# Optimization experiments

Hardware: AMD Instinct MI355X
Metric: run time of the kernel (lower is better)

Reference implementation:

```python
import jax, jax.numpy as jnp
import numpy as np

DIM = 512
HEADS = 8
DIM_HEAD = 64
INNER = HEADS * DIM_HEAD
SCALE = DIM_HEAD ** -0.5


def setup_inputs() -> dict:
    key = jax.random.key(0)
    ks = jax.random.split(key, 6)
    b, n = 2, 2048
    x = jax.random.normal(ks[0], (b, n, DIM), dtype=jnp.float32)
    # torch Linear(dim, 3*inner, bias=False): store as [in, out] for x @ W
    w_qkv = jax.random.normal(ks[1], (DIM, 3 * INNER), dtype=jnp.float32) * (DIM ** -0.5)
    # Conv2d(heads, heads, 1, bias=False) weights squeezed to [out_h, in_h]
    w_pre = jax.random.normal(ks[2], (HEADS, HEADS), dtype=jnp.float32) * (HEADS ** -0.5)
    w_post = jax.random.normal(ks[3], (HEADS, HEADS), dtype=jnp.float32) * (HEADS ** -0.5)
    w_out = jax.random.normal(ks[4], (INNER, DIM), dtype=jnp.float32) * (INNER ** -0.5)
    b_out = jax.random.normal(ks[5], (DIM,), dtype=jnp.float32) * 0.01
    return {"x": x, "w_qkv": w_qkv, "w_pre": w_pre, "w_post": w_post,
            "w_out": w_out, "b_out": b_out}


def reference(x, w_qkv, w_pre, w_post, w_out, b_out):
    b, n, _ = x.shape
    qkv = x @ w_qkv  # [b, n, 3*inner]
    q, k, v = jnp.split(qkv, 3, axis=-1)
    # b n (h d) -> b h n d
    split_heads = lambda t: t.reshape(b, n, HEADS, DIM_HEAD).transpose(0, 2, 1, 3)
    q, k, v = split_heads(q), split_heads(k), split_heads(v)
    dots = jnp.einsum('bhid,bhjd->bhij', q, k) * SCALE
    # pre-softmax talking-heads: 1x1 conv over the head axis
    dots = jnp.einsum('gh,bhij->bgij', w_pre, dots)
    attn = jax.nn.softmax(dots, axis=-1)
    # post-softmax talking-heads mix
    attn = jnp.einsum('gh,bhij->bgij', w_post, attn)
    out = jnp.einsum('bhij,bhjd->bhid', attn, v)
    out = out.transpose(0, 2, 1, 3).reshape(b, n, INNER)  # b h n d -> b n (h d)
    return out @ w_out + b_out
```

## Files before the change

### kernel.cpp

```cpp
#include <hip/hip_runtime.h>
#include <hip/hip_bf16.h>

typedef unsigned short ushort_t;
typedef __attribute__((ext_vector_type(8))) short short8;
typedef __attribute__((ext_vector_type(4))) short short4v;
typedef __attribute__((ext_vector_type(4))) float floatx4;

#define MFMA16(a, b, c) __builtin_amdgcn_mfma_f32_16x16x32_bf16(a, b, c, 0, 0, 0)

__device__ __forceinline__ float bf2f(ushort_t u) {
    unsigned int v = ((unsigned int)u) << 16;
    return __int_as_float((int)v);
}
__device__ __forceinline__ ushort_t f2bf(float f) {
    unsigned int x = (unsigned int)__float_as_int(f);
    unsigned int r = (x + 0x7FFFu + ((x >> 16) & 1u)) >> 16;
    return (ushort_t)r;
}

__global__ __launch_bounds__(256) void k_cvt(const floatx4* __restrict__ src,
                                             short4v* __restrict__ dst, int n4) {
    int i = blockIdx.x * 256 + threadIdx.x;
    if (i < n4) {
        floatx4 v = src[i];
        short4v o;
        o[0] = (short)f2bf(v[0]);
        o[1] = (short)f2bf(v[1]);
        o[2] = (short)f2bf(v[2]);
        o[3] = (short)f2bf(v[3]);
        dst[i] = o;
    }
}

__global__ __launch_bounds__(256) void k_transpose_cvt(const float* __restrict__ src,
                                                       ushort_t* __restrict__ dst, int R, int C) {
    __shared__ float t[32][33];
    int tx = threadIdx.x & 31, ty = threadIdx.x >> 5;
    int r0 = blockIdx.y * 32, c0 = blockIdx.x * 32;
    for (int y = ty; y < 32; y += 8) t[y][tx] = src[(r0 + y) * C + c0 + tx];
    __syncthreads();
    for (int y = ty; y < 32; y += 8) dst[(c0 + y) * R + r0 + tx] = f2bf(t[tx][y]);
}

__global__ __launch_bounds__(256) void k_qkv(const ushort_t* __restrict__ x,
                                             const ushort_t* __restrict__ wt,
                                             ushort_t* __restrict__ qs,
                                             ushort_t* __restrict__ ks,
                                             ushort_t* __restrict__ vt) {
    const int tid = threadIdx.x, lane = tid & 63, wv = tid >> 6;
    const int col = lane & 15, quad = lane >> 4;
    const int row0 = blockIdx.y * 64 + (wv >> 1) * 32;
    const int c0 = blockIdx.x * 64 + (wv & 1) * 32;
    floatx4 acc[2][2];
#pragma unroll
    for (int i = 0; i < 2; i++)
#pragma unroll
        for (int j = 0; j < 2; j++) acc[i][j] = (floatx4){0.f, 0.f, 0.f, 0.f};
    for (int k0 = 0; k0 < 512; k0 += 32) {
        const int ko = k0 + quad * 8;
        short8 a0 = *(const short8*)&x[(row0 + col) * 512 + ko];
        short8 a1 = *(const short8*)&x[(row0 + 16 + col) * 512 + ko];
        short8 b0 = *(const short8*)&wt[(c0 + col) * 512 + ko];
        short8 b1 = *(const short8*)&wt[(c0 + 16 + col) * 512 + ko];
        acc[0][0] = MFMA16(a0, b0, acc[0][0]);
        acc[0][1] = MFMA16(a0, b1, acc[0][1]);
        acc[1][0] = MFMA16(a1, b0, acc[1][0]);
        acc[1][1] = MFMA16(a1, b1, acc[1][1]);
    }
#pragma unroll
    for (int i = 0; i < 2; i++)
#pragma unroll
        for (int j = 0; j < 2; j++)
#pragma unroll
            for (int r = 0; r < 4; r++) {
                int row = row0 + i * 16 + quad * 4 + r;
                int c = c0 + j * 16 + col;
                float v = acc[i][j][r];
                int bb = row >> 11, n = row & 2047;
                int which = c >> 9, hh = (c >> 6) & 7, d = c & 63;
                int hidx = bb * 8 + hh;
                if (which == 0)
                    qs[(hidx * 2048 + n) * 64 + d] = f2bf(v * 0.125f);
                else if (which == 1)
                    ks[(hidx * 2048 + n) * 64 + d] = f2bf(v);
                else
                    vt[(hidx * 64 + d) * 2048 + n] = f2bf(v);
            }
}

__global__ __launch_bounds__(512) void k_attn(const ushort_t* __restrict__ qs,
                                              const ushort_t* __restrict__ ks,
                                              const ushort_t* __restrict__ vt,
                                              const float* __restrict__ w_pre,
                                              const float* __restrict__ w_post,
                                              const ushort_t* __restrict__ wot,
                                              const float* __restrict__ bias,
                                              float* __restrict__ out) {
    __shared__ __align__(16) ushort_t qlds[8 * 16 * 72];
    __shared__ __align__(16) ushort_t amix[8 * 16 * 136];
    __shared__ __align__(16) ushort_t oline[16 * 520];
    __shared__ float wbuf[128];
    __shared__ float red[8][8][16][2];
    __shared__ float clds[8][16];
    const int tid = threadIdx.x, lane = tid & 63, wv = tid >> 6;
    const int col = lane & 15, quad = lane >> 4;
    const int b = blockIdx.y, n0 = blockIdx.x * 16;

    if (tid < 64) wbuf[tid] = w_pre[tid];
    else if (tid < 128) wbuf[tid] = w_post[tid - 64];
    for (int c = tid; c < 1024; c += 512) {
        int hh = c >> 7, rem = c & 127, ii = rem >> 3, dc = (rem & 7) * 8;
        *(short8*)&qlds[(hh * 16 + ii) * 72 + dc] =
            *(const short8*)&qs[((b * 8 + hh) * 2048 + n0 + ii) * 64 + dc];
    }
    __syncthreads();

    float M[8][4], L[8][4];
#pragma unroll
    for (int g = 0; g < 8; g++)
#pragma unroll
        for (int r = 0; r < 4; r++) { M[g][r] = -1e30f; L[g][r] = 0.f; }
    for (int jt = 0; jt < 16; jt++) {
        const int jw = jt * 128 + wv * 16;
        floatx4 S[8];
#pragma unroll
        for (int h = 0; h < 8; h++) {
            const ushort_t* qb = &qlds[(h * 16 + col) * 72 + quad * 8];
            short8 a0 = *(const short8*)&qb[0];
            short8 a1 = *(const short8*)&qb[32];
            const ushort_t* kb = &ks[((b * 8 + h) * 2048 + jw + col) * 64 + quad * 8];
            short8 b0 = *(const short8*)&kb[0];
            short8 b1 = *(const short8*)&kb[32];
            floatx4 a = (floatx4){0.f, 0.f, 0.f, 0.f};
            a = MFMA16(a0, b0, a);
            a = MFMA16(a1, b1, a);
            S[h] = a;
        }
#pragma unroll
        for (int g = 0; g < 8; g++)
#pragma unroll
            for (int r = 0; r < 4; r++) {
                float s = 0.f;
#pragma unroll
                for (int h = 0; h < 8; h++) s = fmaf(wbuf[g * 8 + h], S[h][r], s);
                float Mn = fmaxf(M[g][r], s);
                L[g][r] = L[g][r] * __expf(M[g][r] - Mn) + __expf(s - Mn);
                M[g][r] = Mn;
            }
    }
#pragma unroll
    for (int g = 0; g < 8; g++)
#pragma unroll
        for (int r = 0; r < 4; r++) {
            float M0 = M[g][r], L0 = L[g][r];
#pragma unroll
            for (int k = 1; k < 16; k <<= 1) {
                float Mo = __shfl_xor(M0, k, 64);
                float Lo = __shfl_xor(L0, k, 64);
                float Mn = fmaxf(M0, Mo);
                L0 = L0 * __expf(M0 - Mn) + Lo * __expf(Mo - Mn);
                M0 = Mn;
            }
            if (col == 0) { red[wv][g][quad * 4 + r][0] = M0; red[wv][g][quad * 4 + r][1] = L0; }
        }
    __syncthreads();
    if (tid < 128) {
        int g = tid >> 4, ii = tid & 15;
        float m = -1e30f;
#pragma unroll
        for (int w2 = 0; w2 < 8; w2++) m = fmaxf(m, red[w2][g][ii][0]);
        float l = 0.f;
#pragma unroll
        for (int w2 = 0; w2 < 8; w2++) l += red[w2][g][ii][1] * __expf(red[w2][g][ii][0] - m);
        clds[g][ii] = m + __logf(fmaxf(l, 1e-30f));
    }
    __syncthreads();
    float cr[8][4];
#pragma unroll
    for (int g = 0; g < 8; g++)
#pragma unroll
        for (int r = 0; r < 4; r++) cr[g][r] = clds[g][quad * 4 + r];

    floatx4 O[4];
#pragma unroll
    for (int nt = 0; nt < 4; nt++) O[nt] = (floatx4){0.f, 0.f, 0.f, 0.f};
    const int e = wv;
    for (int jt = 0; jt < 16; jt++) {
        const int j0 = jt * 128;
        const int jw = j0 + wv * 16;
        floatx4 S[8];
#pragma unroll
        for (int h = 0; h < 8; h++) {
            const ushort_t* qb = &qlds[(h * 16 + col) * 72 + quad * 8];
            short8 a0 = *(const short8*)&qb[0];
            short8 a1 = *(const short8*)&qb[32];
            const ushort_t* kb = &ks[((b * 8 + h) * 2048 + jw + col) * 64 + quad * 8];
            short8 b0 = *(const short8*)&kb[0];
            short8 b1 = *(const short8*)&kb[32];
            floatx4 a = (floatx4){0.f, 0.f, 0.f, 0.f};
            a = MFMA16(a0, b0, a);
            a = MFMA16(a1, b1, a);
            S[h] = a;
        }
        float P[8][4];
#pragma unroll
        for (int g = 0; g < 8; g++)
#pragma unroll
            for (int r = 0; r < 4; r++) {
                float s = 0.f;
#pragma unroll
                for (int h = 0; h < 8; h++) s = fmaf(wbuf[g * 8 + h], S[h][r], s);
                P[g][r] = __expf(fminf(s - cr[g][r], 30.f));
            }
#pragma unroll
        for (int e2 = 0; e2 < 8; e2++)
#pragma unroll
            for (int r = 0; r < 4; r++) {
                float a = 0.f;
#pragma unroll
                for (int g = 0; g < 8; g++) a = fmaf(wbuf[64 + e2 * 8 + g], P[g][r], a);
                amix[(e2 * 16 + quad * 4 + r) * 136 + wv * 16 + col] = f2bf(a);
            }
        __syncthreads();
#pragma unroll
        for (int nt = 0; nt < 4; nt++) {
            floatx4 a = O[nt];
#pragma unroll
            for (int k2 = 0; k2 < 4; k2++) {
                short8 af = *(const short8*)&amix[(e * 16 + col) * 136 + k2 * 32 + quad * 8];
                short8 bf = *(const short8*)&vt[((b * 8 + e) * 64 + nt * 16 + col) * 2048 + j0 +
                                                k2 * 32 + quad * 8];
                a = MFMA16(af, bf, a);
            }
            O[nt] = a;
        }
        __syncthreads();
    }
#pragma unroll
    for (int nt = 0; nt < 4; nt++)
#pragma unroll
        for (int r = 0; r < 4; r++)
            oline[(quad * 4 + r) * 520 + e * 64 + nt * 16 + col] = f2bf(O[nt][r]);
    __syncthreads();
#pragma unroll
    for (int nt = 0; nt < 4; nt++) {
        floatx4 acc = (floatx4){0.f, 0.f, 0.f, 0.f};
        const int c = wv * 64 + nt * 16 + col;
#pragma unroll
        for (int k2 = 0; k2 < 16; k2++) {
            short8 af = *(const short8*)&oline[col * 520 + k2 * 32 + quad * 8];
            short8 bf = *(const short8*)&wot[c * 512 + k2 * 32 + quad * 8];
            acc = MFMA16(af, bf, acc);
        }
        float bz = bias[c];
#pragma unroll
        for (int r = 0; r < 4; r++)
            out[(b * 2048 + n0 + quad * 4 + r) * 512 + c] = acc[r] + bz;
    }
}

extern "C" void kernel_launch(void* const* d_in, const int* in_sizes, int n_in,
                              void* d_out, int out_size, void* d_ws, size_t ws_size,
                              hipStream_t stream) {
    const float* x = (const float*)d_in[0];
    const float* w_qkv = (const float*)d_in[1];
    const float* w_pre = (const float*)d_in[2];
    const float* w_post = (const float*)d_in[3];
    const float* w_out = (const float*)d_in[4];
    const float* b_out = (const float*)d_in[5];
    char* ws = (char*)d_ws;
    ushort_t* qs = (ushort_t*)(ws);
    ushort_t* ks = (ushort_t*)(ws + (4u << 20));
    ushort_t* vt = (ushort_t*)(ws + (8u << 20));
    ushort_t* xb = (ushort_t*)(ws + (12u << 20));
    ushort_t* wt = (ushort_t*)(ws + (16u << 20));
    ushort_t* wot = (ushort_t*)(ws + (16u << 20) + 1572864u);
    float* out = (float*)d_out;

    k_cvt<<<dim3(2048), dim3(256), 0, stream>>>((const floatx4*)x, (short4v*)xb, 524288);
    k_transpose_cvt<<<dim3(48, 16), dim3(256), 0, stream>>>(w_qkv, wt, 512, 1536);
    k_transpose_cvt<<<dim3(16, 16), dim3(256), 0, stream>>>(w_out, wot, 512, 512);
    k_qkv<<<dim3(24, 64), dim3(256), 0, stream>>>(xb, wt, qs, ks, vt);
    k_attn<<<dim3(128, 2), dim3(512), 0, stream>>>(qs, ks, vt, w_pre, w_post, wot, b_out, out);
}
```

Before: 358.3 us.

## Single-pass attention without max subtraction; defer post-mix and normalization to end

The attention kernel drops the two-pass softmax (a stats pass, then a recompute pass) and makes one pass. It accumulates unnormalized exp(s) times V for every pre-mixed head g on the MFMA units, then applies the post-softmax head mix and the 1/L normalization once at the end. This removes the second QK^T recompute and the per-tile post-mix, at the cost of 32 accumulator tiles per wave and no max subtraction, which risks overflow for large logits. The QKV projection kernel now stages its tile in LDS and writes coalesced 16-byte rows, including the transposed V layout. The attention kernel's launch bounds are also tightened.

```diff
diff --git a/kernel.cpp b/kernel.cpp
--- a/kernel.cpp
+++ b/kernel.cpp
@@ -47,10 +47,15 @@
                                              ushort_t* __restrict__ qs,
                                              ushort_t* __restrict__ ks,
                                              ushort_t* __restrict__ vt) {
+    __shared__ __align__(16) ushort_t st[64 * 72];
     const int tid = threadIdx.x, lane = tid & 63, wv = tid >> 6;
     const int col = lane & 15, quad = lane >> 4;
     const int row0 = blockIdx.y * 64 + (wv >> 1) * 32;
     const int c0 = blockIdx.x * 64 + (wv & 1) * 32;
+    const int which = blockIdx.x >> 3, hh = blockIdx.x & 7;
+    const int brow0 = blockIdx.y * 64;
+    const int bb = brow0 >> 11, n0 = brow0 & 2047;
+    const int hidx = bb * 8 + hh;
     floatx4 acc[2][2];
 #pragma unroll
     for (int i = 0; i < 2; i++)
@@ -67,44 +72,54 @@
         acc[1][0] = MFMA16(a1, b0, acc[1][0]);
         acc[1][1] = MFMA16(a1, b1, acc[1][1]);
     }
+    const float qscale = (which == 0) ? 0.125f : 1.0f;
 #pragma unroll
     for (int i = 0; i < 2; i++)
 #pragma unroll
         for (int j = 0; j < 2; j++)
 #pragma unroll
             for (int r = 0; r < 4; r++) {
-                int row = row0 + i * 16 + quad * 4 + r;
-                int c = c0 + j * 16 + col;
-                float v = acc[i][j][r];
-                int bb = row >> 11, n = row & 2047;
-                int which = c >> 9, hh = (c >> 6) & 7, d = c & 63;
-                int hidx = bb * 8 + hh;
-                if (which == 0)
-                    qs[(hidx * 2048 + n) * 64 + d] = f2bf(v * 0.125f);
-                else if (which == 1)
-                    ks[(hidx * 2048 + n) * 64 + d] = f2bf(v);
-                else
-                    vt[(hidx * 64 + d) * 2048 + n] = f2bf(v);
+                int il = (wv >> 1) * 32 + i * 16 + quad * 4 + r;
+                int cl = (wv & 1) * 32 + j * 16 + col;
+                ushort_t hv = f2bf(acc[i][j][r] * qscale);
+                if (which == 2) st[cl * 72 + il] = hv;
+                else            st[il * 72 + cl] = hv;
             }
-}
-
-__global__ __launch_bounds__(512) void k_attn(const ushort_t* __restrict__ qs,
-                                              const ushort_t* __restrict__ ks,
-                                              const ushort_t* __restrict__ vt,
-                                              const float* __restrict__ w_pre,
-                                              const float* __restrict__ w_post,
-                                              const ushort_t* __restrict__ wot,
-                                              const float* __restrict__ bias,
-                                              float* __restrict__ out) {
+    __syncthreads();
+    if (which < 2) {
+        ushort_t* dst = (which == 0) ? qs : ks;
+#pragma unroll
+        for (int s = tid; s < 512; s += 256) {
+            int rr = s >> 3, dc = (s & 7) * 8;
+            *(short8*)&dst[(hidx * 2048 + n0 + rr) * 64 + dc] = *(const short8*)&st[rr * 72 + dc];
+        }
+    } else {
+#pragma unroll
+        for (int s = tid; s < 512; s += 256) {
+            int d = s >> 3, nc = (s & 7) * 8;
+            *(short8*)&vt[(hidx * 64 + d) * 2048 + n0 + nc] = *(const short8*)&st[d * 72 + nc];
+        }
+    }
+}
+
+__global__ __launch_bounds__(512, 2) void k_attn(const ushort_t* __restrict__ qs,
+                                                 const ushort_t* __restrict__ ks,
+                                                 const ushort_t* __restrict__ vt,
+                                                 const float* __restrict__ w_pre,
+                                                 const float* __restrict__ w_post,
+                                                 const ushort_t* __restrict__ wot,
+                                                 const float* __restrict__ bias,
+                                                 float* __restrict__ out) {
     __shared__ __align__(16) ushort_t qlds[8 * 16 * 72];
-    __shared__ __align__(16) ushort_t amix[8 * 16 * 136];
+    __shared__ __align__(16) ushort_t U[8 * 16 * 136];
     __shared__ __align__(16) ushort_t oline[16 * 520];
     __shared__ float wbuf[128];
-    __shared__ float red[8][8][16][2];
-    __shared__ float clds[8][16];
+    __shared__ float lred[8][8][16];
+    __shared__ float linv[8][16];
     const int tid = threadIdx.x, lane = tid & 63, wv = tid >> 6;
     const int col = lane & 15, quad = lane >> 4;
     const int b = blockIdx.y, n0 = blockIdx.x * 16;
+    const int e = wv;
 
     if (tid < 64) wbuf[tid] = w_pre[tid];
     else if (tid < 128) wbuf[tid] = w_post[tid - 64];
@@ -115,13 +130,19 @@
     }
     __syncthreads();
 
-    float M[8][4], L[8][4];
-#pragma unroll
-    for (int g = 0; g < 8; g++)
-#pragma unroll
-        for (int r = 0; r < 4; r++) { M[g][r] = -1e30f; L[g][r] = 0.f; }
+    float Lacc[8][4];
+    floatx4 Oa[8][4];
+#pragma unroll
+    for (int g = 0; g < 8; g++) {
+#pragma unroll
+        for (int r = 0; r < 4; r++) Lacc[g][r] = 0.f;
+#pragma unroll
+        for (int nt = 0; nt < 4; nt++) Oa[g][nt] = (floatx4){0.f, 0.f, 0.f, 0.f};
+    }
+
     for (int jt = 0; jt < 16; jt++) {
-        const int jw = jt * 128 + wv * 16;
+        const int j0 = jt * 128;
+        const int jw = j0 + wv * 16;
         floatx4 S[8];
 #pragma unroll
         for (int h = 0; h < 8; h++) {
@@ -143,104 +164,66 @@
                 float s = 0.f;
 #pragma unroll
                 for (int h = 0; h < 8; h++) s = fmaf(wbuf[g * 8 + h], S[h][r], s);
-                float Mn = fmaxf(M[g][r], s);
-                L[g][r] = L[g][r] * __expf(M[g][r] - Mn) + __expf(s - Mn);
-                M[g][r] = Mn;
+                float u = __expf(s);
+                Lacc[g][r] += u;
+                U[(g * 16 + quad * 4 + r) * 136 + wv * 16 + col] = f2bf(u);
             }
-    }
+        __syncthreads();
+#pragma unroll
+        for (int k2 = 0; k2 < 4; k2++) {
+            short8 bf[4];
+#pragma unroll
+            for (int nt = 0; nt < 4; nt++)
+                bf[nt] = *(const short8*)&vt[((b * 8 + e) * 64 + nt * 16 + col) * 2048 + j0 +
+                                             k2 * 32 + quad * 8];
+            short8 af[8];
+#pragma unroll
+            for (int g = 0; g < 8; g++)
+                af[g] = *(const short8*)&U[(g * 16 + col) * 136 + k2 * 32 + quad * 8];
+#pragma unroll
+            for (int g = 0; g < 8; g++)
+#pragma unroll
+                for (int nt = 0; nt < 4; nt++) Oa[g][nt] = MFMA16(af[g], bf[nt], Oa[g][nt]);
+        }
+        __syncthreads();
+    }
+
 #pragma unroll
     for (int g = 0; g < 8; g++)
 #pragma unroll
         for (int r = 0; r < 4; r++) {
-            float M0 = M[g][r], L0 = L[g][r];
-#pragma unroll
-            for (int k = 1; k < 16; k <<= 1) {
-                float Mo = __shfl_xor(M0, k, 64);
-                float Lo = __shfl_xor(L0, k, 64);
-                float Mn = fmaxf(M0, Mo);
-                L0 = L0 * __expf(M0 - Mn) + Lo * __expf(Mo - Mn);
-                M0 = Mn;
-            }
-            if (col == 0) { red[wv][g][quad * 4 + r][0] = M0; red[wv][g][quad * 4 + r][1] = L0; }
+            float v = Lacc[g][r];
+            v += __shfl_xor(v, 1, 64);
+            v += __shfl_xor(v, 2, 64);
+            v += __shfl_xor(v, 4, 64);
+            v += __shfl_xor(v, 8, 64);
+            if (col == 0) lred[wv][g][quad * 4 + r] = v;
         }
     __syncthreads();
     if (tid < 128) {
         int g = tid >> 4, ii = tid & 15;
-        float m = -1e30f;
-#pragma unroll
-        for (int w2 = 0; w2 < 8; w2++) m = fmaxf(m, red[w2][g][ii][0]);
         float l = 0.f;
 #pragma unroll
-        for (int w2 = 0; w2 < 8; w2++) l += red[w2][g][ii][1] * __expf(red[w2][g][ii][0] - m);
-        clds[g][ii] = m + __logf(fmaxf(l, 1e-30f));
-    }
-    __syncthreads();
-    float cr[8][4];
-#pragma unroll
-    for (int g = 0; g < 8; g++)
-#pragma unroll
-        for (int r = 0; r < 4; r++) cr[g][r] = clds[g][quad * 4 + r];
-
-    floatx4 O[4];
-#pragma unroll
-    for (int nt = 0; nt < 4; nt++) O[nt] = (floatx4){0.f, 0.f, 0.f, 0.f};
-    const int e = wv;
-    for (int jt = 0; jt < 16; jt++) {
-        const int j0 = jt * 128;
-        const int jw = j0 + wv * 16;
-        floatx4 S[8];
-#pragma unroll
-        for (int h = 0; h < 8; h++) {
-            const ushort_t* qb = &qlds[(h * 16 + col) * 72 + quad * 8];
-            short8 a0 = *(const short8*)&qb[0];
-            short8 a1 = *(const short8*)&qb[32];
-            const ushort_t* kb = &ks[((b * 8 + h) * 2048 + jw + col) * 64 + quad * 8];
-            short8 b0 = *(const short8*)&kb[0];
-            short8 b1 = *(const short8*)&kb[32];
-            floatx4 a = (floatx4){0.f, 0.f, 0.f, 0.f};
-            a = MFMA16(a0, b0, a);
-            a = MFMA16(a1, b1, a);
-            S[h] = a;
-        }
-        float P[8][4];
-#pragma unroll
-        for (int g = 0; g < 8; g++)
-#pragma unroll
-            for (int r = 0; r < 4; r++) {
-                float s = 0.f;
-#pragma unroll
-                for (int h = 0; h < 8; h++) s = fmaf(wbuf[g * 8 + h], S[h][r], s);
-                P[g][r] = __expf(fminf(s - cr[g][r], 30.f));
-            }
-#pragma unroll
-        for (int e2 = 0; e2 < 8; e2++)
-#pragma unroll
-            for (int r = 0; r < 4; r++) {
-                float a = 0.f;
-#pragma unroll
-                for (int g = 0; g < 8; g++) a = fmaf(wbuf[64 + e2 * 8 + g], P[g][r], a);
-                amix[(e2 * 16 + quad * 4 + r) * 136 + wv * 16 + col] = f2bf(a);
-            }
-        __syncthreads();
-#pragma unroll
-        for (int nt = 0; nt < 4; nt++) {
-            floatx4 a = O[nt];
-#pragma unroll
-            for (int k2 = 0; k2 < 4; k2++) {
-                short8 af = *(const short8*)&amix[(e * 16 + col) * 136 + k2 * 32 + quad * 8];
-                short8 bf = *(const short8*)&vt[((b * 8 + e) * 64 + nt * 16 + col) * 2048 + j0 +
-                                                k2 * 32 + quad * 8];
-                a = MFMA16(af, bf, a);
-            }
-            O[nt] = a;
-        }
-        __syncthreads();
+        for (int w2 = 0; w2 < 8; w2++) l += lred[w2][g][ii];
+        linv[g][ii] = 1.0f / l;
+    }
+    __syncthreads();
+    float coef[8][4];
+#pragma unroll
+    for (int g = 0; g < 8; g++) {
+        float wqe = wbuf[64 + e * 8 + g];
+#pragma unroll
+        for (int r = 0; r < 4; r++) coef[g][r] = wqe * linv[g][quad * 4 + r];
     }
 #pragma unroll
     for (int nt = 0; nt < 4; nt++)
 #pragma unroll
-        for (int r = 0; r < 4; r++)
-            oline[(quad * 4 + r) * 520 + e * 64 + nt * 16 + col] = f2bf(O[nt][r]);
+        for (int r = 0; r < 4; r++) {
+            float o = 0.f;
+#pragma unroll
+            for (int g = 0; g < 8; g++) o = fmaf(coef[g][r], Oa[g][nt][r], o);
+            oline[(quad * 4 + r) * 520 + e * 64 + nt * 16 + col] = f2bf(o);
+        }
     __syncthreads();
 #pragma unroll
     for (int nt = 0; nt < 4; nt++) {
```

After: 308.3 us. -14.0%, faster.
